# Optimization experiments

Hardware: AMD Instinct MI355X
Metric: run time of the kernel (lower is better)

Reference implementation:

```python
import jax, jax.numpy as jnp
import numpy as np

WINDOW = 11
CHANNEL = 3
SIGMA = 1.5


def _gaussian_kernel():
    coords = jnp.arange(WINDOW, dtype=jnp.float32) - (WINDOW - 1) / 2.0
    g = jnp.exp(-(coords ** 2) / (2.0 * SIGMA ** 2))
    g = g / g.sum()
    k2d = g[:, None] * g[None, :]                      # (k, k)
    # depthwise kernel, OIHW with feature_group_count=C -> (C, 1, k, k)
    return jnp.tile(k2d[None, None], (CHANNEL, 1, 1, 1))


def _dwconv(x, kernel):
    pad = WINDOW // 2
    return jax.lax.conv_general_dilated(
        x, kernel, window_strides=(1, 1),
        padding=((pad, pad), (pad, pad)),
        dimension_numbers=("NCHW", "OIHW", "NCHW"),
        feature_group_count=CHANNEL)


def setup_inputs() -> dict:
    key = jax.random.key(0)
    k1, k2 = jax.random.split(key)
    B, C, H, W = 32, 3, 512, 512
    denoised = jax.random.uniform(k1, (B, C, H, W), dtype=jnp.float32)
    clean = jax.random.uniform(k2, (B, C, H, W), dtype=jnp.float32)
    return {"denoised": denoised, "clean": clean}


def reference(denoised, clean):
    kernel = _gaussian_kernel()
    img1 = jnp.clip(denoised, 0.0, 1.0)
    img2 = jnp.clip(clean, 0.0, 1.0)

    mu1 = _dwconv(img1, kernel)
    mu2 = _dwconv(img2, kernel)
    mu1_sq = mu1 * mu1
    mu2_sq = mu2 * mu2
    mu1_mu2 = mu1 * mu2
    sigma1_sq = _dwconv(img1 * img1, kernel) - mu1_sq
    sigma2_sq = _dwconv(img2 * img2, kernel) - mu2_sq
    sigma12 = _dwconv(img1 * img2, kernel) - mu1_mu2

    C1 = 0.01 ** 2
    C2 = 0.03 ** 2
    ssim_map = ((2.0 * mu1_mu2 + C1) * (2.0 * sigma12 + C2)) / (
        (mu1_sq + mu2_sq + C1) * (sigma1_sq + sigma2_sq + C2))
    return 1.0 - ssim_map.mean()
```

## Files before the change

### kernel.cpp

```cpp
#include <hip/hip_runtime.h>

#define IMG_H 512
#define IMG_W 512
#define TILE_COLS 256
#define TILE_ROWS 8
#define HALO 5
#define VCOLS (TILE_COLS + 2*HALO)
#define NTHREADS 256
#define VSTRIDE2 272
#define NROWS_IN (TILE_ROWS + 2*HALO)
#define NCH 4
#define NSLOTS 64

typedef _Float16 h2 __attribute__((ext_vector_type(2)));

#define W0 0.00102838f
#define W1 0.00759876f
#define W2 0.03600077f
#define W3 0.10936053f
#define W4 0.21300556f
#define W5 0.26601170f

static constexpr float GW[11] = { W0,W1,W2,W3,W4,W5,W4,W3,W2,W1,W0 };

static __device__ const h2 WEVEN[6] = {
    {(_Float16)W0,(_Float16)W1},{(_Float16)W2,(_Float16)W3},{(_Float16)W4,(_Float16)W5},
    {(_Float16)W4,(_Float16)W3},{(_Float16)W2,(_Float16)W1},{(_Float16)W0,(_Float16)0.f}
};
static __device__ const h2 WODD[6] = {
    {(_Float16)0.f,(_Float16)W0},{(_Float16)W1,(_Float16)W2},{(_Float16)W3,(_Float16)W4},
    {(_Float16)W5,(_Float16)W4},{(_Float16)W3,(_Float16)W2},{(_Float16)W1,(_Float16)W0}
};

__device__ __forceinline__ void hconv4h(const _Float16* __restrict__ pp, float out[4]) {
    union { uint2 u2[4]; h2 p[8]; _Float16 h[16]; } w;
#pragma unroll
    for (int v = 0; v < 4; ++v) w.u2[v] = *(const uint2*)(pp + 4*v);
#if __has_builtin(__builtin_amdgcn_fdot2)
#pragma unroll
    for (int o = 0; o < 4; ++o) {
        const int base = o >> 1;
        float s = 0.f;
        if (o & 1) {
#pragma unroll
            for (int t = 0; t < 6; ++t)
                s = __builtin_amdgcn_fdot2(w.p[base + t], WODD[t], s, false);
        } else {
#pragma unroll
            for (int t = 0; t < 6; ++t)
                s = __builtin_amdgcn_fdot2(w.p[base + t], WEVEN[t], s, false);
        }
        out[o] = s;
    }
#else
    float f[16];
#pragma unroll
    for (int i = 0; i < 16; ++i) f[i] = (float)w.h[i];
#pragma unroll
    for (int o = 0; o < 4; ++o) {
        float s = 0.f;
#pragma unroll
        for (int t = 0; t < 11; ++t) s = fmaf(GW[t], f[o+t], s);
        out[o] = s;
    }
#endif
}

__device__ __forceinline__ void vertical_col(
    int v, int c0, int y0, size_t pbase,
    const float* __restrict__ den, const float* __restrict__ cln,
    _Float16 (*vbuf)[TILE_ROWS][VSTRIDE2]) {
    const int gc = c0 - HALO + v;
    const bool colok = (gc >= 0) && (gc < IMG_W);

    float xv[NROWS_IN], yv[NROWS_IN];
#pragma unroll
    for (int i = 0; i < NROWS_IN; ++i) {
        const int gr = y0 - HALO + i;
        const bool ok = colok && ((unsigned)gr < (unsigned)IMG_H);
        float x = 0.f, y = 0.f;
        if (ok) {
            const size_t idx = pbase + (size_t)gr * IMG_W + gc;
            x = den[idx]; y = cln[idx];
        }
        xv[i] = x; yv[i] = y;
    }

    float a0[TILE_ROWS], a1[TILE_ROWS], a2[TILE_ROWS], a3[TILE_ROWS];
#pragma unroll
    for (int r = 0; r < TILE_ROWS; ++r) { a0[r]=a1[r]=a2[r]=a3[r]=0.f; }
#pragma unroll
    for (int i = 0; i < NROWS_IN; ++i) {
        const float x = fminf(fmaxf(xv[i], 0.f), 1.f);
        const float y = fminf(fmaxf(yv[i], 0.f), 1.f);
        const float q = fmaf(x, x, y * y);
        const float p = x * y;
#pragma unroll
        for (int r = 0; r < TILE_ROWS; ++r) {
            const int t = i - r;
            if (t >= 0 && t <= 10) {
                const float w = GW[t];
                a0[r] = fmaf(w, x, a0[r]);
                a1[r] = fmaf(w, y, a1[r]);
                a2[r] = fmaf(w, q, a2[r]);
                a3[r] = fmaf(w, p, a3[r]);
            }
        }
    }
#pragma unroll
    for (int r = 0; r < TILE_ROWS; ++r) {
        vbuf[0][r][v] = (_Float16)a0[r];
        vbuf[1][r][v] = (_Float16)a1[r];
        vbuf[2][r][v] = (_Float16)a2[r];
        vbuf[3][r][v] = (_Float16)a3[r];
    }
}

__global__ __launch_bounds__(NTHREADS, 4)
void ssim_fused(const float* __restrict__ den, const float* __restrict__ cln,
                double* __restrict__ slots) {
    __shared__ __align__(16) _Float16 vbuf[NCH][TILE_ROWS][VSTRIDE2];
    __shared__ float red[NTHREADS/64];

    const int tid = threadIdx.x;
    const int b  = blockIdx.x;
    const int cs    = b & 1;
    const int rs    = (b >> 1) & 63;
    const int plane = b >> 7;

    const int c0 = cs * TILE_COLS;
    const int y0 = rs * TILE_ROWS;
    const size_t pbase = (size_t)plane * (IMG_H * IMG_W);

    vertical_col(tid, c0, y0, pbase, den, cln, vbuf);
    if (tid < VCOLS - NTHREADS)
        vertical_col(NTHREADS + tid, c0, y0, pbase, den, cln, vbuf);
    __syncthreads();

    float ssim_acc = 0.f;
#pragma unroll
    for (int s = 0; s < 2; ++s) {
        const int item = tid + NTHREADS * s;
        const int row = item >> 6;
        const int j4  = (item & 63) << 2;
        float bx[4], by[4], bq[4], bp[4];
        hconv4h(&vbuf[0][row][j4], bx);
        hconv4h(&vbuf[1][row][j4], by);
        hconv4h(&vbuf[2][row][j4], bq);
        hconv4h(&vbuf[3][row][j4], bp);
#pragma unroll
        for (int o = 0; o < 4; ++o) {
            const float C1 = 1e-4f, C2 = 9e-4f;
            const float mu1 = bx[o], mu2 = by[o];
            const float mu1s = mu1*mu1, mu2s = mu2*mu2, mu12 = mu1*mu2;
            const float ssum = bq[o] - mu1s - mu2s;
            const float s12  = bp[o] - mu12;
            const float num = fmaf(2.f, mu12, C1) * fmaf(2.f, s12, C2);
            const float dnm = (mu1s + mu2s + C1) * (ssum + C2);
            ssim_acc = fmaf(num, __builtin_amdgcn_rcpf(dnm), ssim_acc);
        }
    }

#pragma unroll
    for (int off = 32; off > 0; off >>= 1)
        ssim_acc += __shfl_down(ssim_acc, off, 64);
    if ((tid & 63) == 0) red[tid >> 6] = ssim_acc;
    __syncthreads();
    if (tid == 0) {
        const float s = red[0] + red[1] + red[2] + red[3];
        atomicAdd(&slots[(size_t)(b & (NSLOTS - 1)) * 8], (double)s);
    }
}

__global__ void ssim_finalize(const double* __restrict__ slots, float* __restrict__ out,
                              double inv_n) {
    double s = 0.0;
    for (int i = 0; i < NSLOTS; ++i) s += slots[i * 8];
    out[0] = 1.0f - (float)(s * inv_n);
}

extern "C" void kernel_launch(void* const* d_in, const int* in_sizes, int n_in,
                              void* d_out, int out_size, void* d_ws, size_t ws_size,
                              hipStream_t stream) {
    const float* den = (const float*)d_in[0];
    const float* cln = (const float*)d_in[1];
    float* out = (float*)d_out;
    double* slots = (double*)d_ws;

    hipMemsetAsync(d_ws, 0, NSLOTS * 64, stream);

    const int n = in_sizes[0];
    const int planes = n / (IMG_H * IMG_W);
    dim3 grid(planes * 2 * 64);
    ssim_fused<<<grid, NTHREADS, 0, stream>>>(den, cln, slots);
    ssim_finalize<<<1, 1, 0, stream>>>(slots, out, 1.0 / (double)n);
}
```

Before: 296.3 us.

## Compute separable Gaussian SSIM convolutions with MFMA banded-matrix multiplies

Recasts both the vertical and horizontal 11-tap Gaussian passes as 16x16x32 f16 MFMA multiplies against a banded weight matrix, replacing the scalar FMA vertical pass and fdot2 horizontal pass. The four SSIM channels are staged in fp16 in swizzled shared memory, and the tiles change to 16x128 outputs. Blocks are remapped so neighbouring launches touch different planes and rows. Tile overlap now re-reads a 26/16 halo of rows, and the clipped inputs go through fp16 before the vertical pass, which reduces precision.

Result: slower. 337.3 us (+13.8%).

```diff
diff --git a/kernel.cpp b/kernel.cpp
--- a/kernel.cpp
+++ b/kernel.cpp
@@ -1,187 +1,185 @@
 #include <hip/hip_runtime.h>
 
-#define IMG_H 512
-#define IMG_W 512
-#define TILE_COLS 256
-#define TILE_ROWS 8
+#define IMG 512
+#define OUT_R 16
+#define OUT_C 128
 #define HALO 5
-#define VCOLS (TILE_COLS + 2*HALO)
-#define NTHREADS 256
-#define VSTRIDE2 272
-#define NROWS_IN (TILE_ROWS + 2*HALO)
-#define NCH 4
+#define IN_R 26
+#define IN_C 138
+#define CPAD 144
+#define VS 152
+#define NT 256
 #define NSLOTS 64
 
-typedef _Float16 h2 __attribute__((ext_vector_type(2)));
+typedef _Float16 f16x8 __attribute__((ext_vector_type(8)));
+typedef float    f32x4 __attribute__((ext_vector_type(4)));
 
-#define W0 0.00102838f
-#define W1 0.00759876f
-#define W2 0.03600077f
-#define W3 0.10936053f
-#define W4 0.21300556f
-#define W5 0.26601170f
+static constexpr float GWf[11] = {
+    0.00102838f, 0.00759876f, 0.03600077f, 0.10936053f, 0.21300556f,
+    0.26601170f, 0.21300556f, 0.10936053f, 0.03600077f, 0.00759876f,
+    0.00102838f };
 
-static constexpr float GW[11] = { W0,W1,W2,W3,W4,W5,W4,W3,W2,W1,W0 };
+struct WTab { alignas(16) _Float16 v[4][16][8]; };
+static constexpr WTab make_wtab() {
+    WTab t{};
+    for (int g = 0; g < 4; ++g)
+        for (int j = 0; j < 16; ++j)
+            for (int b = 0; b < 8; ++b) {
+                const int d = 8 * g + b - j;
+                t.v[g][j][b] = (d >= 0 && d <= 10) ? (_Float16)GWf[d]
+                                                   : (_Float16)0.f;
+            }
+    return t;
+}
+__device__ constexpr WTab WTAB = make_wtab();
 
-static __device__ const h2 WEVEN[6] = {
-    {(_Float16)W0,(_Float16)W1},{(_Float16)W2,(_Float16)W3},{(_Float16)W4,(_Float16)W5},
-    {(_Float16)W4,(_Float16)W3},{(_Float16)W2,(_Float16)W1},{(_Float16)W0,(_Float16)0.f}
+union SMem {
+    _Float16 ch[4][CPAD][32];
+    _Float16 vb[4][OUT_R][VS];
 };
-static __device__ const h2 WODD[6] = {
-    {(_Float16)0.f,(_Float16)W0},{(_Float16)W1,(_Float16)W2},{(_Float16)W3,(_Float16)W4},
-    {(_Float16)W5,(_Float16)W4},{(_Float16)W3,(_Float16)W2},{(_Float16)W1,(_Float16)W0}
-};
+static_assert(sizeof(SMem) == 4 * CPAD * 32 * 2, "smem size");
 
-__device__ __forceinline__ void hconv4h(const _Float16* __restrict__ pp, float out[4]) {
-    union { uint2 u2[4]; h2 p[8]; _Float16 h[16]; } w;
+__device__ __forceinline__ void prep_task(int task, int c0, int y0,
+                                          size_t pbase,
+                                          const float* __restrict__ den,
+                                          const float* __restrict__ cln,
+                                          SMem* sm) {
+    const int rh = (task >= CPAD) ? 1 : 0;
+    const int c  = task - CPAD * rh;
+    const int gc = c0 - HALO + c;
+    const bool colok = ((unsigned)gc < IMG) && (c < IN_C);
+    union { f16x8 v8[8]; _Float16 h[64]; } st;
+    const int r0 = rh * 16;
 #pragma unroll
-    for (int v = 0; v < 4; ++v) w.u2[v] = *(const uint2*)(pp + 4*v);
-#if __has_builtin(__builtin_amdgcn_fdot2)
-#pragma unroll
-    for (int o = 0; o < 4; ++o) {
-        const int base = o >> 1;
-        float s = 0.f;
-        if (o & 1) {
-#pragma unroll
-            for (int t = 0; t < 6; ++t)
-                s = __builtin_amdgcn_fdot2(w.p[base + t], WODD[t], s, false);
-        } else {
-#pragma unroll
-            for (int t = 0; t < 6; ++t)
-                s = __builtin_amdgcn_fdot2(w.p[base + t], WEVEN[t], s, false);
-        }
-        out[o] = s;
-    }
-#else
-    float f[16];
-#pragma unroll
-    for (int i = 0; i < 16; ++i) f[i] = (float)w.h[i];
-#pragma unroll
-    for (int o = 0; o < 4; ++o) {
-        float s = 0.f;
-#pragma unroll
-        for (int t = 0; t < 11; ++t) s = fmaf(GW[t], f[o+t], s);
-        out[o] = s;
-    }
-#endif
-}
-
-__device__ __forceinline__ void vertical_col(
-    int v, int c0, int y0, size_t pbase,
-    const float* __restrict__ den, const float* __restrict__ cln,
-    _Float16 (*vbuf)[TILE_ROWS][VSTRIDE2]) {
-    const int gc = c0 - HALO + v;
-    const bool colok = (gc >= 0) && (gc < IMG_W);
-
-    float xv[NROWS_IN], yv[NROWS_IN];
-#pragma unroll
-    for (int i = 0; i < NROWS_IN; ++i) {
-        const int gr = y0 - HALO + i;
-        const bool ok = colok && ((unsigned)gr < (unsigned)IMG_H);
+    for (int rr = 0; rr < 16; ++rr) {
+        const int R  = r0 + rr;
+        const int gr = y0 - HALO + R;
         float x = 0.f, y = 0.f;
-        if (ok) {
-            const size_t idx = pbase + (size_t)gr * IMG_W + gc;
+        if (colok && ((unsigned)gr < IMG) && (R < IN_R)) {
+            const size_t idx = pbase + (size_t)gr * IMG + gc;
             x = den[idx]; y = cln[idx];
         }
-        xv[i] = x; yv[i] = y;
+        x = fminf(fmaxf(x, 0.f), 1.f);
+        y = fminf(fmaxf(y, 0.f), 1.f);
+        st.h[rr]      = (_Float16)x;
+        st.h[16 + rr] = (_Float16)y;
+        st.h[32 + rr] = (_Float16)fmaf(x, x, y * y);
+        st.h[48 + rr] = (_Float16)(x * y);
     }
-
-    float a0[TILE_ROWS], a1[TILE_ROWS], a2[TILE_ROWS], a3[TILE_ROWS];
+    const int sw = (c >> 1) & 3;
 #pragma unroll
-    for (int r = 0; r < TILE_ROWS; ++r) { a0[r]=a1[r]=a2[r]=a3[r]=0.f; }
+    for (int ch = 0; ch < 4; ++ch) {
 #pragma unroll
-    for (int i = 0; i < NROWS_IN; ++i) {
-        const float x = fminf(fmaxf(xv[i], 0.f), 1.f);
-        const float y = fminf(fmaxf(yv[i], 0.f), 1.f);
-        const float q = fmaf(x, x, y * y);
-        const float p = x * y;
-#pragma unroll
-        for (int r = 0; r < TILE_ROWS; ++r) {
-            const int t = i - r;
-            if (t >= 0 && t <= 10) {
-                const float w = GW[t];
-                a0[r] = fmaf(w, x, a0[r]);
-                a1[r] = fmaf(w, y, a1[r]);
-                a2[r] = fmaf(w, q, a2[r]);
-                a3[r] = fmaf(w, p, a3[r]);
-            }
+        for (int gg = 0; gg < 2; ++gg) {
+            const int g = rh * 2 + gg;
+            *reinterpret_cast<f16x8*>(&sm->ch[ch][c][(g ^ sw) * 8]) =
+                st.v8[ch * 2 + gg];
         }
-    }
-#pragma unroll
-    for (int r = 0; r < TILE_ROWS; ++r) {
-        vbuf[0][r][v] = (_Float16)a0[r];
-        vbuf[1][r][v] = (_Float16)a1[r];
-        vbuf[2][r][v] = (_Float16)a2[r];
-        vbuf[3][r][v] = (_Float16)a3[r];
     }
 }
 
-__global__ __launch_bounds__(NTHREADS, 4)
-void ssim_fused(const float* __restrict__ den, const float* __restrict__ cln,
-                double* __restrict__ slots) {
-    __shared__ __align__(16) _Float16 vbuf[NCH][TILE_ROWS][VSTRIDE2];
-    __shared__ float red[NTHREADS/64];
+__global__ __launch_bounds__(NT, 4)
+void ssim_mfma(const float* __restrict__ den, const float* __restrict__ cln,
+               double* __restrict__ slots) {
+    __shared__ SMem sm;
+    __shared__ float red[NT / 64];
 
-    const int tid = threadIdx.x;
-    const int b  = blockIdx.x;
-    const int cs    = b & 1;
-    const int rs    = (b >> 1) & 63;
-    const int plane = b >> 7;
+    const int t    = threadIdx.x;
+    const int lane = t & 63;
+    const int w    = t >> 6;
+    const int fj   = lane & 15;
+    const int fg   = lane >> 4;
 
-    const int c0 = cs * TILE_COLS;
-    const int y0 = rs * TILE_ROWS;
-    const size_t pbase = (size_t)plane * (IMG_H * IMG_W);
+    const int bid = blockIdx.x;
+    int vid = bid;
+    if ((gridDim.x & 7) == 0) {
+        const int chunk = gridDim.x >> 3;
+        vid = (bid & 7) * chunk + (bid >> 3);
+    }
+    const int rs    = vid & 31;
+    const int cs    = (vid >> 5) & 3;
+    const int plane = vid >> 7;
+    const int c0 = cs * OUT_C;
+    const int y0 = rs * OUT_R;
+    const size_t pbase = (size_t)plane * (IMG * IMG);
 
-    vertical_col(tid, c0, y0, pbase, den, cln, vbuf);
-    if (tid < VCOLS - NTHREADS)
-        vertical_col(NTHREADS + tid, c0, y0, pbase, den, cln, vbuf);
+    const f16x8 wf = *reinterpret_cast<const f16x8*>(WTAB.v[fg][fj]);
+
+    prep_task(t, c0, y0, pbase, den, cln, &sm);
+    if (t < 2 * CPAD - NT)
+        prep_task(NT + t, c0, y0, pbase, den, cln, &sm);
     __syncthreads();
 
-    float ssim_acc = 0.f;
+    const f32x4 zero4 = {0.f, 0.f, 0.f, 0.f};
+    f32x4 acc[9];
 #pragma unroll
-    for (int s = 0; s < 2; ++s) {
-        const int item = tid + NTHREADS * s;
-        const int row = item >> 6;
-        const int j4  = (item & 63) << 2;
-        float bx[4], by[4], bq[4], bp[4];
-        hconv4h(&vbuf[0][row][j4], bx);
-        hconv4h(&vbuf[1][row][j4], by);
-        hconv4h(&vbuf[2][row][j4], bq);
-        hconv4h(&vbuf[3][row][j4], bp);
+    for (int n = 0; n < 9; ++n) {
+        const int tau  = 9 * w + n;
+        const int tile = tau >> 2;
+        const int ch   = tau & 3;
+        const int colp = tile * 16 + fj;
+        const f16x8 bf = *reinterpret_cast<const f16x8*>(
+            &sm.ch[ch][colp][(fg ^ ((colp >> 1) & 3)) * 8]);
+        acc[n] = __builtin_amdgcn_mfma_f32_16x16x32_f16(wf, bf, zero4, 0, 0, 0);
+    }
+    __syncthreads();
 #pragma unroll
-        for (int o = 0; o < 4; ++o) {
+    for (int n = 0; n < 9; ++n) {
+        const int tau  = 9 * w + n;
+        const int tile = tau >> 2;
+        const int ch   = tau & 3;
+#pragma unroll
+        for (int b = 0; b < 4; ++b)
+            sm.vb[ch][4 * fg + b][tile * 16 + fj] = (_Float16)acc[n][b];
+    }
+    __syncthreads();
+
+    float sacc = 0.f;
+#pragma unroll
+    for (int mt = 0; mt < 2; ++mt) {
+        const int m = 2 * w + mt;
+        f32x4 d[4];
+#pragma unroll
+        for (int ch = 0; ch < 4; ++ch) {
+            const f16x8 af = *reinterpret_cast<const f16x8*>(
+                &sm.vb[ch][fj][m * 16 + 8 * fg]);
+            d[ch] = __builtin_amdgcn_mfma_f32_16x16x32_f16(af, wf, zero4, 0, 0, 0);
+        }
+#pragma unroll
+        for (int b = 0; b < 4; ++b) {
             const float C1 = 1e-4f, C2 = 9e-4f;
-            const float mu1 = bx[o], mu2 = by[o];
-            const float mu1s = mu1*mu1, mu2s = mu2*mu2, mu12 = mu1*mu2;
-            const float ssum = bq[o] - mu1s - mu2s;
-            const float s12  = bp[o] - mu12;
-            const float num = fmaf(2.f, mu12, C1) * fmaf(2.f, s12, C2);
-            const float dnm = (mu1s + mu2s + C1) * (ssum + C2);
-            ssim_acc = fmaf(num, __builtin_amdgcn_rcpf(dnm), ssim_acc);
+            const float mu1 = d[0][b], mu2 = d[1][b];
+            const float qb  = d[2][b], pb  = d[3][b];
+            const float mu1s = mu1 * mu1, mu2s = mu2 * mu2, mu12 = mu1 * mu2;
+            const float ssum = qb - mu1s - mu2s;
+            const float s12  = pb - mu12;
+            const float num  = fmaf(2.f, mu12, C1) * fmaf(2.f, s12, C2);
+            const float dnm  = (mu1s + mu2s + C1) * (ssum + C2);
+            sacc = fmaf(num, __builtin_amdgcn_rcpf(dnm), sacc);
         }
     }
 
 #pragma unroll
     for (int off = 32; off > 0; off >>= 1)
-        ssim_acc += __shfl_down(ssim_acc, off, 64);
-    if ((tid & 63) == 0) red[tid >> 6] = ssim_acc;
+        sacc += __shfl_down(sacc, off, 64);
+    if (lane == 0) red[w] = sacc;
     __syncthreads();
-    if (tid == 0) {
+    if (t == 0) {
         const float s = red[0] + red[1] + red[2] + red[3];
-        atomicAdd(&slots[(size_t)(b & (NSLOTS - 1)) * 8], (double)s);
+        atomicAdd(&slots[(size_t)(bid & (NSLOTS - 1)) * 8], (double)s);
     }
 }
 
-__global__ void ssim_finalize(const double* __restrict__ slots, float* __restrict__ out,
-                              double inv_n) {
+__global__ void ssim_finalize(const double* __restrict__ slots,
+                              float* __restrict__ out, double inv_n) {
     double s = 0.0;
     for (int i = 0; i < NSLOTS; ++i) s += slots[i * 8];
     out[0] = 1.0f - (float)(s * inv_n);
 }
 
 extern "C" void kernel_launch(void* const* d_in, const int* in_sizes, int n_in,
-                              void* d_out, int out_size, void* d_ws, size_t ws_size,
-                              hipStream_t stream) {
+                              void* d_out, int out_size, void* d_ws,
+                              size_t ws_size, hipStream_t stream) {
     const float* den = (const float*)d_in[0];
     const float* cln = (const float*)d_in[1];
     float* out = (float*)d_out;
@@ -190,8 +188,8 @@
     hipMemsetAsync(d_ws, 0, NSLOTS * 64, stream);
 
     const int n = in_sizes[0];
-    const int planes = n / (IMG_H * IMG_W);
-    dim3 grid(planes * 2 * 64);
-    ssim_fused<<<grid, NTHREADS, 0, stream>>>(den, cln, slots);
+    const int planes = n / (IMG * IMG);
+    dim3 grid(planes * (IMG / OUT_R) * (IMG / OUT_C));
+    ssim_mfma<<<grid, NT, 0, stream>>>(den, cln, slots);
     ssim_finalize<<<1, 1, 0, stream>>>(slots, out, 1.0 / (double)n);
 }
```
